# Kernel tuning notes

Measured on AMD Instinct MI355X. Metric: run time of the kernel, lower is better.

The kernel has to match this reference:

```python
import jax, jax.numpy as jnp
import numpy as np

EMBED_DIM = 1024
NUM_HEADS = 16
HEAD_DIM = EMBED_DIM // NUM_HEADS
SCALING = HEAD_DIM ** -0.5


def setup_inputs() -> dict:
    key = jax.random.key(0)
    ks = jax.random.split(key, 9)
    T, B, E = 2048, 4, EMBED_DIM
    s = 0.02
    return {
        "query": jax.random.normal(ks[0], (T, B, E), dtype=jnp.float32),
        "Wq": jax.random.normal(ks[1], (E, E), dtype=jnp.float32) * s,
        "bq": jnp.zeros((E,), dtype=jnp.float32),
        "Wk": jax.random.normal(ks[2], (E, E), dtype=jnp.float32) * s,
        "bk": jnp.zeros((E,), dtype=jnp.float32),
        "Wv": jax.random.normal(ks[3], (E, E), dtype=jnp.float32) * s,
        "bv": jnp.zeros((E,), dtype=jnp.float32),
        "Wo": jax.random.normal(ks[4], (E, E), dtype=jnp.float32) * s,
        "bo": jnp.zeros((E,), dtype=jnp.float32),
    }


def reference(query, Wq, bq, Wk, bk, Wv, bv, Wo, bo):
    # query: [T, B, E]; torch Linear: x @ W.T + b
    T, B, E = query.shape
    H, D = NUM_HEADS, HEAD_DIM
    q = (query @ Wq.T + bq) * SCALING
    k = query @ Wk.T + bk
    v = query @ Wv.T + bv
    # [T, B, E] -> [B*H, T, D]
    def split_heads(x):
        return x.reshape(T, B * H, D).transpose(1, 0, 2)
    q, k, v = split_heads(q), split_heads(k), split_heads(v)
    attn_weights = jnp.einsum("btd,bsd->bts", q, k)  # [B*H, T, T]
    attn_probs = jax.nn.softmax(attn_weights, axis=-1)
    attn = jnp.einsum("bts,bsd->btd", attn_probs, v)  # [B*H, T, D]
    attn = attn.transpose(1, 0, 2).reshape(T, B, E)
    return attn @ Wo.T + bo
```

## Files before the change

kernel.cpp:

```cpp
#include <hip/hip_runtime.h>
#include <stdint.h>

#define TSEQ   2048
#define BATCH  4
#define NHEAD  16
#define HDIM   64
#define EMB    1024
#define MROWS  (TSEQ * BATCH)
#define QKV_N  (3 * EMB)
#define SCALE_Q 0.125f
#define LOG2E  1.4426950408889634f

typedef __bf16  bf16x8  __attribute__((ext_vector_type(8)));
typedef __bf16  bf16x2  __attribute__((ext_vector_type(2)));
typedef short   s16x8   __attribute__((ext_vector_type(8)));
typedef float   f32x4   __attribute__((ext_vector_type(4)));
typedef float   f32x16  __attribute__((ext_vector_type(16)));

__device__ __forceinline__ uint16_t b16c(float f) {
    __bf16 h = (__bf16)f;
    return __builtin_bit_cast(uint16_t, h);
}
__device__ __forceinline__ uint32_t pk2(float a, float b) {
    bf16x2 h; h[0] = (__bf16)a; h[1] = (__bf16)b;
    return __builtin_bit_cast(uint32_t, h);
}
__device__ __forceinline__ float exp2hw(float x) {
    float r; asm("v_exp_f32 %0, %1" : "=v"(r) : "v"(x)); return r;
}
__device__ __forceinline__ bf16x8 ldfrag(const uint16_t* p) {
    return __builtin_bit_cast(bf16x8, *(const s16x8*)p);
}
__device__ __forceinline__ f32x4 MFMA(bf16x8 a, bf16x8 b, f32x4 c) {
    return __builtin_amdgcn_mfma_f32_16x16x32_bf16(a, b, c, 0, 0, 0);
}
__device__ __forceinline__ f32x16 MFMA32(bf16x8 a, bf16x8 b, f32x16 c) {
    return __builtin_amdgcn_mfma_f32_32x32x16_bf16(a, b, c, 0, 0, 0);
}

#define GLOAD_LDS16(g, l) \
    __builtin_amdgcn_global_load_lds((const __attribute__((address_space(1))) void*)(g), \
                                     (__attribute__((address_space(3))) void*)(l), 16, 0, 0)

__global__ void cvt_f2b4(const float* __restrict__ src, uint16_t* __restrict__ dst, int n4) {
    int i = blockIdx.x * blockDim.x + threadIdx.x;
    if (i >= n4) return;
    float4 v = ((const float4*)src)[i];
    ushort4 o;
    o.x = b16c(v.x); o.y = b16c(v.y); o.z = b16c(v.z); o.w = b16c(v.w);
    ((ushort4*)dst)[i] = o;
}

__global__ void cvt_wqkv(const float* __restrict__ Wq, const float* __restrict__ Wk,
                         const float* __restrict__ Wv, const float* __restrict__ bq,
                         const float* __restrict__ bk, const float* __restrict__ bv,
                         uint16_t* __restrict__ Wqkv, float* __restrict__ bqkv, int n4) {
    int i = blockIdx.x * blockDim.x + threadIdx.x;
    if (i < QKV_N) {
        float bval;
        if (i < EMB)            bval = bq[i] * SCALE_Q;
        else if (i < 2 * EMB)   bval = bk[i - EMB];
        else                    bval = bv[i - 2 * EMB];
        bqkv[i] = bval;
    }
    if (i >= n4) return;
    int e = i * 4;
    int n = e >> 10;
    int k = e & 1023;
    const float* src; float sc;
    if (n < EMB)            { src = Wq + ((size_t)n << 10) + k;             sc = SCALE_Q; }
    else if (n < 2 * EMB)   { src = Wk + ((size_t)(n - EMB) << 10) + k;     sc = 1.f; }
    else                    { src = Wv + ((size_t)(n - 2 * EMB) << 10) + k; sc = 1.f; }
    float4 v = *(const float4*)src;
    ushort4 o;
    o.x = b16c(v.x * sc); o.y = b16c(v.y * sc); o.z = b16c(v.z * sc); o.w = b16c(v.w * sc);
    ((ushort4*)Wqkv)[i] = o;
}

template <typename CT>
__global__ __launch_bounds__(256) void gemm_bt(
        const uint16_t* __restrict__ A, const uint16_t* __restrict__ Bt,
        const float* __restrict__ bias, CT* __restrict__ C,
        int M, int N, int K, int tiles_n) {
    __shared__ uint16_t As[128 * 32];
    __shared__ uint16_t Bs[128 * 32];

    const int nwg = gridDim.x;
    const int bid0 = blockIdx.x;
    const int bid = (bid0 & 7) * (nwg >> 3) + (bid0 >> 3);
    const int tm = bid / tiles_n, tn = bid % tiles_n;
    const int tid = threadIdx.x;
    const int l = tid & 63, w = tid >> 6;
    const int wm = w >> 1, wn = w & 1;
    const int fr = l & 15, fq = l >> 4;

    f32x4 acc[4][4] = {};

    const int row_a = tid >> 2;
    const int kblk  = (tid & 3) << 3;
    const uint16_t* gA0 = A  + (size_t)(tm * 128 + row_a) * K + kblk;
    const uint16_t* gB0 = Bt + (size_t)(tn * 128 + row_a) * K + kblk;
    const uint16_t* gA1 = gA0 + (size_t)64 * K;
    const uint16_t* gB1 = gB0 + (size_t)64 * K;
    uint16_t* lA0 = As + w * 512;
    uint16_t* lA1 = As + 2048 + w * 512;
    uint16_t* lB0 = Bs + w * 512;
    uint16_t* lB1 = Bs + 2048 + w * 512;

    for (int k0 = 0; k0 < K; k0 += 32) {
        GLOAD_LDS16(gA0 + k0, lA0);
        GLOAD_LDS16(gA1 + k0, lA1);
        GLOAD_LDS16(gB0 + k0, lB0);
        GLOAD_LDS16(gB1 + k0, lB1);
        __syncthreads();

        bf16x8 a[4], b[4];
#pragma unroll
        for (int i = 0; i < 4; i++)
            a[i] = ldfrag(&As[(wm * 64 + i * 16 + fr) * 32 + fq * 8]);
#pragma unroll
        for (int i = 0; i < 4; i++)
            b[i] = ldfrag(&Bs[(wn * 64 + i * 16 + fr) * 32 + fq * 8]);
#pragma unroll
        for (int i = 0; i < 4; i++)
#pragma unroll
            for (int j = 0; j < 4; j++)
                acc[i][j] = MFMA(a[i], b[j], acc[i][j]);
        __syncthreads();
    }

#pragma unroll
    for (int j = 0; j < 4; j++) {
        const int col = tn * 128 + wn * 64 + j * 16 + fr;
        const float bv = bias[col];
#pragma unroll
        for (int i = 0; i < 4; i++) {
#pragma unroll
            for (int r = 0; r < 4; r++) {
                const int row = tm * 128 + wm * 64 + i * 16 + fq * 4 + r;
                const float v = acc[i][j][r] + bv;
                if constexpr (sizeof(CT) == 2) C[(size_t)row * N + col] = (CT)b16c(v);
                else                           C[(size_t)row * N + col] = (CT)v;
            }
        }
    }
}

__device__ __forceinline__ int swze(int row, int colE) {
    return (row << 6) + (colE ^ ((((row & 7) ^ ((row >> 3) & 7)) & 7) << 3));
}

__global__ __launch_bounds__(256) void flash_attn2(
        const uint16_t* __restrict__ qkv, uint16_t* __restrict__ attnb) {
    __shared__ __align__(16) uint16_t smem[16384];
    uint16_t* Ks = smem;
    uint16_t* Vt = smem + 4096;

    int bid = (int)blockIdx.x;
    bid = ((bid & 7) << 7) + (bid >> 3);
    const int head = bid >> 4;
    const int qt   = bid & 15;
    const int b    = head >> 4, h = head & 15;
    const int tid  = threadIdx.x;
    const int l  = tid & 63, w = tid >> 6;
    const int q5 = l & 31;
    const int hi = l >> 5;

    const int qrow = qt * 128 + w * 32 + q5;
    const uint16_t* qb = qkv + ((size_t)(qrow * 4 + b)) * 3072 + h * 64 + hi * 8;
    bf16x8 qf[4];
#pragma unroll
    for (int s = 0; s < 4; s++) qf[s] = ldfrag(qb + 16 * s);

    const int sk = tid >> 2;
    const int sc = (tid & 3) * 16;
    const size_t tstep = (size_t)64 * 4 * 3072;
    const uint16_t* kvp = qkv + ((size_t)(sk * 4 + b)) * 3072 + 1024 + h * 64 + sc;

    {
        uint4 k0 = *(const uint4*)(kvp);
        uint4 k1 = *(const uint4*)(kvp + 8);
        uint4 v0 = *(const uint4*)(kvp + 1024);
        uint4 v1 = *(const uint4*)(kvp + 1032);
        kvp += tstep;
        *(uint4*)&Ks[swze(sk, sc)]     = k0;
        *(uint4*)&Ks[swze(sk, sc + 8)] = k1;
        const uint16_t* ve0 = (const uint16_t*)&v0;
        const uint16_t* ve1 = (const uint16_t*)&v1;
#pragma unroll
        for (int j = 0; j < 8; j++) Vt[swze(sc + j, sk)]     = ve0[j];
#pragma unroll
        for (int j = 0; j < 8; j++) Vt[swze(sc + 8 + j, sk)] = ve1[j];
    }
    __syncthreads();

    f32x16 o0 = {}, o1 = {};
    float mrun = -1e30f, lrun = 0.f;

    for (int t = 0; t < 32; t++) {
        uint4 nk0, nk1, nv0, nv1;
        if (t < 31) {
            nk0 = *(const uint4*)(kvp);
            nk1 = *(const uint4*)(kvp + 8);
            nv0 = *(const uint4*)(kvp + 1024);
            nv1 = *(const uint4*)(kvp + 1032);
            kvp += tstep;
        }

        f32x16 s0 = {}, s1 = {};
#pragma unroll
        for (int s = 0; s < 4; s++) {
            bf16x8 kf0 = ldfrag(&Ks[swze(q5,      16 * s + 8 * hi)]);
            bf16x8 kf1 = ldfrag(&Ks[swze(32 + q5, 16 * s + 8 * hi)]);
            s0 = MFMA32(kf0, qf[s], s0);
            s1 = MFMA32(kf1, qf[s], s1);
        }

        float t0 = s0[0], t1 = s0[1], t2 = s0[2], t3 = s0[3];
#pragma unroll
        for (int i = 4; i < 16; i += 4) {
            t0 = fmaxf(t0, s0[i]);     t1 = fmaxf(t1, s0[i + 1]);
            t2 = fmaxf(t2, s0[i + 2]); t3 = fmaxf(t3, s0[i + 3]);
        }
#pragma unroll
        for (int i = 0; i < 16; i += 4) {
            t0 = fmaxf(t0, s1[i]);     t1 = fmaxf(t1, s1[i + 1]);
            t2 = fmaxf(t2, s1[i + 2]); t3 = fmaxf(t3, s1[i + 3]);
        }
        float mx = fmaxf(fmaxf(t0, t1), fmaxf(t2, t3));
        {
            auto rm = __builtin_amdgcn_permlane32_swap(__float_as_int(mx), __float_as_int(mx), false, false);
            mx = fmaxf(__int_as_float(rm[0]), __int_as_float(rm[1]));
        }
        if (!__all(mx <= mrun + 8.f)) {
            float mnew = fmaxf(mrun, mx);
            float scl = exp2hw((mrun - mnew) * LOG2E);
            mrun = mnew;
            lrun *= scl;
#pragma unroll
            for (int i = 0; i < 16; i++) { o0[i] *= scl; o1[i] *= scl; }
        }
        const float mm = mrun * LOG2E;
#pragma unroll
        for (int i = 0; i < 16; i++) s0[i] = exp2hw(__builtin_fmaf(s0[i], LOG2E, -mm));
#pragma unroll
        for (int i = 0; i < 16; i++) s1[i] = exp2hw(__builtin_fmaf(s1[i], LOG2E, -mm));
        float p0 = 0.f, p1 = 0.f, p2 = 0.f, p3 = 0.f;
#pragma unroll
        for (int i = 0; i < 16; i += 4) {
            p0 += s0[i]; p1 += s0[i + 1]; p2 += s0[i + 2]; p3 += s0[i + 3];
            p0 += s1[i]; p1 += s1[i + 1]; p2 += s1[i + 2]; p3 += s1[i + 3];
        }
        float rs = (p0 + p1) + (p2 + p3);
        {
            auto rr2 = __builtin_amdgcn_permlane32_swap(__float_as_int(rs), __float_as_int(rs), false, false);
            rs = __int_as_float(rr2[0]) + __int_as_float(rr2[1]);
        }
        lrun += rs;

        uint32_t pk[16];
#pragma unroll
        for (int rr = 0; rr < 8; rr++) {
            pk[rr]     = pk2(s0[2 * rr], s0[2 * rr + 1]);
            pk[8 + rr] = pk2(s1[2 * rr], s1[2 * rr + 1]);
        }
        bf16x8 pf[4];
#pragma unroll
        for (int kt = 0; kt < 4; kt++) {
            const int b0 = (kt >> 1) * 8 + (kt & 1) * 4;
            auto r02 = __builtin_amdgcn_permlane32_swap((int)pk[b0 + 0], (int)pk[b0 + 2], false, false);
            auto r13 = __builtin_amdgcn_permlane32_swap((int)pk[b0 + 1], (int)pk[b0 + 3], false, false);
            union { uint32_t u[4]; bf16x8 v; } cv;
            cv.u[0] = (uint32_t)r02[0]; cv.u[1] = (uint32_t)r13[0];
            cv.u[2] = (uint32_t)r02[1]; cv.u[3] = (uint32_t)r13[1];
            pf[kt] = cv.v;
        }

#pragma unroll
        for (int kt = 0; kt < 4; kt++) {
            bf16x8 vf0 = ldfrag(&Vt[swze(q5,      16 * kt + 8 * hi)]);
            bf16x8 vf1 = ldfrag(&Vt[swze(32 + q5, 16 * kt + 8 * hi)]);
            o0 = MFMA32(vf0, pf[kt], o0);
            o1 = MFMA32(vf1, pf[kt], o1);
        }

        if (t < 31) {
            __syncthreads();
            *(uint4*)&Ks[swze(sk, sc)]     = nk0;
            *(uint4*)&Ks[swze(sk, sc + 8)] = nk1;
            const uint16_t* ve0 = (const uint16_t*)&nv0;
            const uint16_t* ve1 = (const uint16_t*)&nv1;
#pragma unroll
            for (int j = 0; j < 8; j++) Vt[swze(sc + j, sk)]     = ve0[j];
#pragma unroll
            for (int j = 0; j < 8; j++) Vt[swze(sc + 8 + j, sk)] = ve1[j];
            __syncthreads();
        }
    }

    __syncthreads();
    const float inv = 1.f / lrun;
    uint16_t* Ost = smem + w * 2048;
#pragma unroll
    for (int dt = 0; dt < 2; dt++) {
#pragma unroll
        for (int a = 0; a < 4; a++) {
#pragma unroll
            for (int cp = 0; cp < 2; cp++) {
                const int r = a * 4 + cp * 2;
                float va = (dt ? o1[r] : o0[r]) * inv;
                float vb = (dt ? o1[r + 1] : o0[r + 1]) * inv;
                uint32_t dw = pk2(va, vb);
                const int d0 = dt * 32 + a * 8 + hi * 4 + cp * 2;
                *(uint32_t*)&Ost[swze(q5, d0)] = dw;
            }
        }
    }
    __syncthreads();
    const int rq = l >> 1;
    const int qrow2 = qt * 128 + w * 32 + rq;
    uint16_t* ob = attnb + ((size_t)(qrow2 * 4 + b)) * 1024 + h * 64;
#pragma unroll
    for (int i = 0; i < 4; i++) {
        const int c4 = (l & 1) * 4 + i;
        uint4 vv = *(const uint4*)&Ost[swze(rq, c4 * 8)];
        *(uint4*)(ob + c4 * 8) = vv;
    }
}

extern "C" void kernel_launch(void* const* d_in, const int* in_sizes, int n_in,
                              void* d_out, int out_size, void* d_ws, size_t ws_size,
                              hipStream_t stream) {
    const float* X  = (const float*)d_in[0];
    const float* Wq = (const float*)d_in[1];
    const float* bq = (const float*)d_in[2];
    const float* Wk = (const float*)d_in[3];
    const float* bk = (const float*)d_in[4];
    const float* Wv = (const float*)d_in[5];
    const float* bv = (const float*)d_in[6];
    const float* Wo = (const float*)d_in[7];
    const float* bo = (const float*)d_in[8];
    float* out = (float*)d_out;

    uint8_t* ws = (uint8_t*)d_ws;
    uint16_t* Xbf   = (uint16_t*)(ws);
    uint16_t* Wqkv  = (uint16_t*)(ws + 16777216);
    uint16_t* Wobf  = (uint16_t*)(ws + 23068672);
    float*    bqkv  = (float*)   (ws + 25165824);
    uint16_t* qkv   = (uint16_t*)(ws + 25178112);
    uint16_t* attnb = (uint16_t*)(ws + 75509760);

    cvt_f2b4<<<(MROWS * EMB / 4 + 255) / 256, 256, 0, stream>>>(X, Xbf, MROWS * EMB / 4);
    cvt_f2b4<<<(EMB * EMB / 4 + 255) / 256, 256, 0, stream>>>(Wo, Wobf, EMB * EMB / 4);
    cvt_wqkv<<<(QKV_N * EMB / 4 + 255) / 256, 256, 0, stream>>>(
        Wq, Wk, Wv, bq, bk, bv, Wqkv, bqkv, QKV_N * EMB / 4);

    gemm_bt<uint16_t><<<(MROWS / 128) * (QKV_N / 128), 256, 0, stream>>>(
        Xbf, Wqkv, bqkv, qkv, MROWS, QKV_N, EMB, QKV_N / 128);

    flash_attn2<<<64 * 16, 256, 0, stream>>>(qkv, attnb);

    gemm_bt<float><<<(MROWS / 128) * (EMB / 128), 256, 0, stream>>>(
        attnb, Wobf, bo, out, MROWS, EMB, EMB, EMB / 128);
}
```

Measured before the change: 226.1 us.

## Process two query sub-tiles per wave with double-buffered K/V and direct-to-LDS loads

The attention kernel now gives each wave 64 query rows, held as two 32-row halves, so every K and V fragment read from shared memory feeds twice as many MFMAs. The block count halves to 512. K/V shared buffers are double-buffered so each iteration needs one barrier instead of two. K is loaded with global-to-LDS instructions, and V is transposed with packed 32-bit stores. The cost is higher register pressure from four accumulators and two softmax states, plus fewer blocks to spread across CUs.

Result: faster. 218.6 us (-3.3%).

```diff
diff --git a/kernel.cpp b/kernel.cpp
--- a/kernel.cpp
+++ b/kernel.cpp
@@ -150,181 +150,212 @@
     return (row << 6) + (colE ^ ((((row & 7) ^ ((row >> 3) & 7)) & 7) << 3));
 }
 
-__global__ __launch_bounds__(256) void flash_attn2(
+__device__ __forceinline__ void softmax_half(
+        f32x16& s0, f32x16& s1, float& mrun, float& lrun,
+        f32x16& oa, f32x16& ob, bf16x8* pf) {
+    float t0 = s0[0], t1 = s0[1], t2 = s0[2], t3 = s0[3];
+#pragma unroll
+    for (int i = 4; i < 16; i += 4) {
+        t0 = fmaxf(t0, s0[i]);     t1 = fmaxf(t1, s0[i + 1]);
+        t2 = fmaxf(t2, s0[i + 2]); t3 = fmaxf(t3, s0[i + 3]);
+    }
+#pragma unroll
+    for (int i = 0; i < 16; i += 4) {
+        t0 = fmaxf(t0, s1[i]);     t1 = fmaxf(t1, s1[i + 1]);
+        t2 = fmaxf(t2, s1[i + 2]); t3 = fmaxf(t3, s1[i + 3]);
+    }
+    float mx = fmaxf(fmaxf(t0, t1), fmaxf(t2, t3));
+    {
+        auto rm = __builtin_amdgcn_permlane32_swap(__float_as_int(mx), __float_as_int(mx), false, false);
+        mx = fmaxf(__int_as_float(rm[0]), __int_as_float(rm[1]));
+    }
+    if (!__all(mx <= mrun + 8.f)) {
+        float mnew = fmaxf(mrun, mx);
+        float scl = exp2hw((mrun - mnew) * LOG2E);
+        mrun = mnew;
+        lrun *= scl;
+#pragma unroll
+        for (int i = 0; i < 16; i++) { oa[i] *= scl; ob[i] *= scl; }
+    }
+    const float mm = mrun * LOG2E;
+#pragma unroll
+    for (int i = 0; i < 16; i++) s0[i] = exp2hw(__builtin_fmaf(s0[i], LOG2E, -mm));
+#pragma unroll
+    for (int i = 0; i < 16; i++) s1[i] = exp2hw(__builtin_fmaf(s1[i], LOG2E, -mm));
+    float p0 = 0.f, p1 = 0.f, p2 = 0.f, p3 = 0.f;
+#pragma unroll
+    for (int i = 0; i < 16; i += 4) {
+        p0 += s0[i]; p1 += s0[i + 1]; p2 += s0[i + 2]; p3 += s0[i + 3];
+        p0 += s1[i]; p1 += s1[i + 1]; p2 += s1[i + 2]; p3 += s1[i + 3];
+    }
+    float rs = (p0 + p1) + (p2 + p3);
+    {
+        auto rr2 = __builtin_amdgcn_permlane32_swap(__float_as_int(rs), __float_as_int(rs), false, false);
+        rs = __int_as_float(rr2[0]) + __int_as_float(rr2[1]);
+    }
+    lrun += rs;
+
+    uint32_t pk[16];
+#pragma unroll
+    for (int rr = 0; rr < 8; rr++) {
+        pk[rr]     = pk2(s0[2 * rr], s0[2 * rr + 1]);
+        pk[8 + rr] = pk2(s1[2 * rr], s1[2 * rr + 1]);
+    }
+#pragma unroll
+    for (int kt = 0; kt < 4; kt++) {
+        const int b0 = (kt >> 1) * 8 + (kt & 1) * 4;
+        auto r02 = __builtin_amdgcn_permlane32_swap((int)pk[b0 + 0], (int)pk[b0 + 2], false, false);
+        auto r13 = __builtin_amdgcn_permlane32_swap((int)pk[b0 + 1], (int)pk[b0 + 3], false, false);
+        union { uint32_t u[4]; bf16x8 v; } cv;
+        cv.u[0] = (uint32_t)r02[0]; cv.u[1] = (uint32_t)r13[0];
+        cv.u[2] = (uint32_t)r02[1]; cv.u[3] = (uint32_t)r13[1];
+        pf[kt] = cv.v;
+    }
+}
+
+__global__ __launch_bounds__(256, 2) void flash_attn3(
         const uint16_t* __restrict__ qkv, uint16_t* __restrict__ attnb) {
     __shared__ __align__(16) uint16_t smem[16384];
-    uint16_t* Ks = smem;
-    uint16_t* Vt = smem + 4096;
+    uint16_t* k0p = smem;
+    uint16_t* k1p = smem + 4096;
+    uint16_t* v0p = smem + 8192;
+    uint16_t* v1p = smem + 12288;
 
     int bid = (int)blockIdx.x;
-    bid = ((bid & 7) << 7) + (bid >> 3);
-    const int head = bid >> 4;
-    const int qt   = bid & 15;
+    bid = (bid & 7) * 64 + (bid >> 3);
+    const int head = bid >> 3;
+    const int qt   = bid & 7;
     const int b    = head >> 4, h = head & 15;
     const int tid  = threadIdx.x;
     const int l  = tid & 63, w = tid >> 6;
     const int q5 = l & 31;
     const int hi = l >> 5;
-
-    const int qrow = qt * 128 + w * 32 + q5;
-    const uint16_t* qb = qkv + ((size_t)(qrow * 4 + b)) * 3072 + h * 64 + hi * 8;
-    bf16x8 qf[4];
-#pragma unroll
-    for (int s = 0; s < 4; s++) qf[s] = ldfrag(qb + 16 * s);
-
-    const int sk = tid >> 2;
-    const int sc = (tid & 3) * 16;
     const size_t tstep = (size_t)64 * 4 * 3072;
-    const uint16_t* kvp = qkv + ((size_t)(sk * 4 + b)) * 3072 + 1024 + h * 64 + sc;
-
+
+    const int qrowA = qt * 256 + w * 64 + q5;
+    const uint16_t* qbA = qkv + ((size_t)(qrowA * 4 + b)) * 3072 + h * 64 + hi * 8;
+    const uint16_t* qbB = qbA + (size_t)32 * 4 * 3072;
+    bf16x8 qA[4], qB[4];
+#pragma unroll
+    for (int s = 0; s < 4; s++) { qA[s] = ldfrag(qbA + 16 * s); qB[s] = ldfrag(qbB + 16 * s); }
+
+    const int r0 = w * 16 + (l >> 3);
+    const int r1 = r0 + 8;
+    const int cu0 = (((l & 7) ^ ((r0 & 7) ^ ((r0 >> 3) & 7))) & 7) << 3;
+    const int cu1 = (((l & 7) ^ ((r1 & 7) ^ ((r1 >> 3) & 7))) & 7) << 3;
+    const uint16_t* gk0 = qkv + ((size_t)(r0 * 4 + b)) * 3072 + 1024 + h * 64 + cu0;
+    const uint16_t* gk1 = qkv + ((size_t)(r1 * 4 + b)) * 3072 + 1024 + h * 64 + cu1;
+    const int kdst0 = w * 1024;
+    const int kdst1 = w * 1024 + 512;
+
+    const int skv  = (tid >> 3) * 2;
+    const int scol = (tid & 7) * 8;
+    const uint16_t* gv = qkv + ((size_t)(skv * 4 + b)) * 3072 + 2048 + h * 64 + scol;
+    int voff[8];
+#pragma unroll
+    for (int j2 = 0; j2 < 8; j2++)
+        voff[j2] = (scol + j2) * 64 + (skv ^ ((((j2 ^ (scol >> 3)) & 7)) << 3));
+
+    GLOAD_LDS16(gk0, k0p + kdst0);
+    GLOAD_LDS16(gk1, k0p + kdst1);
     {
-        uint4 k0 = *(const uint4*)(kvp);
-        uint4 k1 = *(const uint4*)(kvp + 8);
-        uint4 v0 = *(const uint4*)(kvp + 1024);
-        uint4 v1 = *(const uint4*)(kvp + 1032);
-        kvp += tstep;
-        *(uint4*)&Ks[swze(sk, sc)]     = k0;
-        *(uint4*)&Ks[swze(sk, sc + 8)] = k1;
-        const uint16_t* ve0 = (const uint16_t*)&v0;
-        const uint16_t* ve1 = (const uint16_t*)&v1;
-#pragma unroll
-        for (int j = 0; j < 8; j++) Vt[swze(sc + j, sk)]     = ve0[j];
-#pragma unroll
-        for (int j = 0; j < 8; j++) Vt[swze(sc + 8 + j, sk)] = ve1[j];
-    }
+        uint4 a0 = *(const uint4*)gv;
+        uint4 a1 = *(const uint4*)(gv + 12288);
+        const uint16_t* e0 = (const uint16_t*)&a0;
+        const uint16_t* e1 = (const uint16_t*)&a1;
+#pragma unroll
+        for (int j2 = 0; j2 < 8; j2++)
+            *(uint32_t*)&v0p[voff[j2]] = (uint32_t)e0[j2] | ((uint32_t)e1[j2] << 16);
+    }
+    gk0 += tstep; gk1 += tstep; gv += tstep;
     __syncthreads();
 
-    f32x16 o0 = {}, o1 = {};
-    float mrun = -1e30f, lrun = 0.f;
+    f32x16 o0 = {}, o1 = {}, o2 = {}, o3 = {};
+    float mrunA = -1e30f, lrunA = 0.f, mrunB = -1e30f, lrunB = 0.f;
 
     for (int t = 0; t < 32; t++) {
-        uint4 nk0, nk1, nv0, nv1;
+        const uint16_t* kb = (t & 1) ? k1p : k0p;
+        const uint16_t* vb = (t & 1) ? v1p : v0p;
+        uint16_t* kn = (t & 1) ? k0p : k1p;
+        uint16_t* vn = (t & 1) ? v0p : v1p;
+
+        uint4 a0, a1;
         if (t < 31) {
-            nk0 = *(const uint4*)(kvp);
-            nk1 = *(const uint4*)(kvp + 8);
-            nv0 = *(const uint4*)(kvp + 1024);
-            nv1 = *(const uint4*)(kvp + 1032);
-            kvp += tstep;
-        }
-
-        f32x16 s0 = {}, s1 = {};
+            GLOAD_LDS16(gk0, kn + kdst0);
+            GLOAD_LDS16(gk1, kn + kdst1);
+            a0 = *(const uint4*)gv;
+            a1 = *(const uint4*)(gv + 12288);
+            gk0 += tstep; gk1 += tstep; gv += tstep;
+        }
+
+        f32x16 sA0 = {}, sA1 = {}, sB0 = {}, sB1 = {};
 #pragma unroll
         for (int s = 0; s < 4; s++) {
-            bf16x8 kf0 = ldfrag(&Ks[swze(q5,      16 * s + 8 * hi)]);
-            bf16x8 kf1 = ldfrag(&Ks[swze(32 + q5, 16 * s + 8 * hi)]);
-            s0 = MFMA32(kf0, qf[s], s0);
-            s1 = MFMA32(kf1, qf[s], s1);
-        }
-
-        float t0 = s0[0], t1 = s0[1], t2 = s0[2], t3 = s0[3];
-#pragma unroll
-        for (int i = 4; i < 16; i += 4) {
-            t0 = fmaxf(t0, s0[i]);     t1 = fmaxf(t1, s0[i + 1]);
-            t2 = fmaxf(t2, s0[i + 2]); t3 = fmaxf(t3, s0[i + 3]);
-        }
-#pragma unroll
-        for (int i = 0; i < 16; i += 4) {
-            t0 = fmaxf(t0, s1[i]);     t1 = fmaxf(t1, s1[i + 1]);
-            t2 = fmaxf(t2, s1[i + 2]); t3 = fmaxf(t3, s1[i + 3]);
-        }
-        float mx = fmaxf(fmaxf(t0, t1), fmaxf(t2, t3));
-        {
-            auto rm = __builtin_amdgcn_permlane32_swap(__float_as_int(mx), __float_as_int(mx), false, false);
-            mx = fmaxf(__int_as_float(rm[0]), __int_as_float(rm[1]));
-        }
-        if (!__all(mx <= mrun + 8.f)) {
-            float mnew = fmaxf(mrun, mx);
-            float scl = exp2hw((mrun - mnew) * LOG2E);
-            mrun = mnew;
-            lrun *= scl;
-#pragma unroll
-            for (int i = 0; i < 16; i++) { o0[i] *= scl; o1[i] *= scl; }
-        }
-        const float mm = mrun * LOG2E;
-#pragma unroll
-        for (int i = 0; i < 16; i++) s0[i] = exp2hw(__builtin_fmaf(s0[i], LOG2E, -mm));
-#pragma unroll
-        for (int i = 0; i < 16; i++) s1[i] = exp2hw(__builtin_fmaf(s1[i], LOG2E, -mm));
-        float p0 = 0.f, p1 = 0.f, p2 = 0.f, p3 = 0.f;
-#pragma unroll
-        for (int i = 0; i < 16; i += 4) {
-            p0 += s0[i]; p1 += s0[i + 1]; p2 += s0[i + 2]; p3 += s0[i + 3];
-            p0 += s1[i]; p1 += s1[i + 1]; p2 += s1[i + 2]; p3 += s1[i + 3];
-        }
-        float rs = (p0 + p1) + (p2 + p3);
-        {
-            auto rr2 = __builtin_amdgcn_permlane32_swap(__float_as_int(rs), __float_as_int(rs), false, false);
-            rs = __int_as_float(rr2[0]) + __int_as_float(rr2[1]);
-        }
-        lrun += rs;
-
-        uint32_t pk[16];
-#pragma unroll
-        for (int rr = 0; rr < 8; rr++) {
-            pk[rr]     = pk2(s0[2 * rr], s0[2 * rr + 1]);
-            pk[8 + rr] = pk2(s1[2 * rr], s1[2 * rr + 1]);
-        }
-        bf16x8 pf[4];
+            bf16x8 kf0 = ldfrag(&kb[swze(q5,      16 * s + 8 * hi)]);
+            bf16x8 kf1 = ldfrag(&kb[swze(32 + q5, 16 * s + 8 * hi)]);
+            sA0 = MFMA32(kf0, qA[s], sA0);
+            sA1 = MFMA32(kf1, qA[s], sA1);
+            sB0 = MFMA32(kf0, qB[s], sB0);
+            sB1 = MFMA32(kf1, qB[s], sB1);
+        }
+
+        bf16x8 pfA[4], pfB[4];
+        softmax_half(sA0, sA1, mrunA, lrunA, o0, o1, pfA);
+        softmax_half(sB0, sB1, mrunB, lrunB, o2, o3, pfB);
+
 #pragma unroll
         for (int kt = 0; kt < 4; kt++) {
-            const int b0 = (kt >> 1) * 8 + (kt & 1) * 4;
-            auto r02 = __builtin_amdgcn_permlane32_swap((int)pk[b0 + 0], (int)pk[b0 + 2], false, false);
-            auto r13 = __builtin_amdgcn_permlane32_swap((int)pk[b0 + 1], (int)pk[b0 + 3], false, false);
-            union { uint32_t u[4]; bf16x8 v; } cv;
-            cv.u[0] = (uint32_t)r02[0]; cv.u[1] = (uint32_t)r13[0];
-            cv.u[2] = (uint32_t)r02[1]; cv.u[3] = (uint32_t)r13[1];
-            pf[kt] = cv.v;
-        }
-
-#pragma unroll
-        for (int kt = 0; kt < 4; kt++) {
-            bf16x8 vf0 = ldfrag(&Vt[swze(q5,      16 * kt + 8 * hi)]);
-            bf16x8 vf1 = ldfrag(&Vt[swze(32 + q5, 16 * kt + 8 * hi)]);
-            o0 = MFMA32(vf0, pf[kt], o0);
-            o1 = MFMA32(vf1, pf[kt], o1);
+            bf16x8 vf0 = ldfrag(&vb[swze(q5,      16 * kt + 8 * hi)]);
+            bf16x8 vf1 = ldfrag(&vb[swze(32 + q5, 16 * kt + 8 * hi)]);
+            o0 = MFMA32(vf0, pfA[kt], o0);
+            o1 = MFMA32(vf1, pfA[kt], o1);
+            o2 = MFMA32(vf0, pfB[kt], o2);
+            o3 = MFMA32(vf1, pfB[kt], o3);
         }
 
         if (t < 31) {
-            __syncthreads();
-            *(uint4*)&Ks[swze(sk, sc)]     = nk0;
-            *(uint4*)&Ks[swze(sk, sc + 8)] = nk1;
-            const uint16_t* ve0 = (const uint16_t*)&nv0;
-            const uint16_t* ve1 = (const uint16_t*)&nv1;
-#pragma unroll
-            for (int j = 0; j < 8; j++) Vt[swze(sc + j, sk)]     = ve0[j];
-#pragma unroll
-            for (int j = 0; j < 8; j++) Vt[swze(sc + 8 + j, sk)] = ve1[j];
-            __syncthreads();
-        }
-    }
-
-    __syncthreads();
-    const float inv = 1.f / lrun;
-    uint16_t* Ost = smem + w * 2048;
-#pragma unroll
-    for (int dt = 0; dt < 2; dt++) {
-#pragma unroll
-        for (int a = 0; a < 4; a++) {
-#pragma unroll
-            for (int cp = 0; cp < 2; cp++) {
-                const int r = a * 4 + cp * 2;
-                float va = (dt ? o1[r] : o0[r]) * inv;
-                float vb = (dt ? o1[r + 1] : o0[r + 1]) * inv;
-                uint32_t dw = pk2(va, vb);
-                const int d0 = dt * 32 + a * 8 + hi * 4 + cp * 2;
-                *(uint32_t*)&Ost[swze(q5, d0)] = dw;
+            const uint16_t* e0 = (const uint16_t*)&a0;
+            const uint16_t* e1 = (const uint16_t*)&a1;
+#pragma unroll
+            for (int j2 = 0; j2 < 8; j2++)
+                *(uint32_t*)&vn[voff[j2]] = (uint32_t)e0[j2] | ((uint32_t)e1[j2] << 16);
+        }
+        __syncthreads();
+    }
+
+    uint16_t* OstA = smem + w * 4096;
+    uint16_t* OstB = OstA + 2048;
+#pragma unroll
+    for (int half = 0; half < 2; half++) {
+        uint16_t* Ost = half ? OstB : OstA;
+        const float inv = 1.f / (half ? lrunB : lrunA);
+#pragma unroll
+        for (int dt = 0; dt < 2; dt++) {
+            const f32x16& ov = half ? (dt ? o3 : o2) : (dt ? o1 : o0);
+#pragma unroll
+            for (int a = 0; a < 4; a++) {
+#pragma unroll
+                for (int cp = 0; cp < 2; cp++) {
+                    const int r = a * 4 + cp * 2;
+                    uint32_t dw = pk2(ov[r] * inv, ov[r + 1] * inv);
+                    const int d0 = dt * 32 + a * 8 + hi * 4 + cp * 2;
+                    *(uint32_t*)&Ost[swze(q5, d0)] = dw;
+                }
             }
         }
     }
-    __syncthreads();
     const int rq = l >> 1;
-    const int qrow2 = qt * 128 + w * 32 + rq;
-    uint16_t* ob = attnb + ((size_t)(qrow2 * 4 + b)) * 1024 + h * 64;
-#pragma unroll
-    for (int i = 0; i < 4; i++) {
-        const int c4 = (l & 1) * 4 + i;
-        uint4 vv = *(const uint4*)&Ost[swze(rq, c4 * 8)];
-        *(uint4*)(ob + c4 * 8) = vv;
+#pragma unroll
+    for (int half = 0; half < 2; half++) {
+        uint16_t* Ost = half ? OstB : OstA;
+        const int qrow2 = qt * 256 + w * 64 + half * 32 + rq;
+        uint16_t* ob = attnb + ((size_t)(qrow2 * 4 + b)) * 1024 + h * 64;
+#pragma unroll
+        for (int i = 0; i < 4; i++) {
+            const int c4 = (l & 1) * 4 + i;
+            uint4 vv = *(const uint4*)&Ost[swze(rq, c4 * 8)];
+            *(uint4*)(ob + c4 * 8) = vv;
+        }
     }
 }
 
@@ -358,7 +389,7 @@
     gemm_bt<uint16_t><<<(MROWS / 128) * (QKV_N / 128), 256, 0, stream>>>(
         Xbf, Wqkv, bqkv, qkv, MROWS, QKV_N, EMB, QKV_N / 128);
 
-    flash_attn2<<<64 * 16, 256, 0, stream>>>(qkv, attnb);
+    flash_attn3<<<512, 256, 0, stream>>>(qkv, attnb);
 
     gemm_bt<float><<<(MROWS / 128) * (EMB / 128), 256, 0, stream>>>(
         attnb, Wobf, bo, out, MROWS, EMB, EMB, EMB / 128);
```
